# Performance work log

Measured on AMD Instinct MI355X. Metric: run time of the kernel, lower is better.

Reference implementation:

```python
import jax, jax.numpy as jnp
import numpy as np

B, C, L = 8, 256, 8192
G, K = 64, 7  # weight channels (groups) and kernel size


def setup_inputs() -> dict:
    key = jax.random.key(0)
    k1, k2 = jax.random.split(key)
    x = jax.random.normal(k1, (B, C, L), dtype=jnp.float32)
    w = jax.random.normal(k2, (B, G, K, L), dtype=jnp.float32)
    return {"x": x, "w": w}


def reference(x, w):
    # x: [B, C, L]; w: [B, G, K, L]
    Bsz, Cin, Len = x.shape
    Gw, Ks = w.shape[1], w.shape[2]
    pad = (Ks - 1) // 2
    x_pad = jnp.pad(x, ((0, 0), (0, 0), (pad, pad)))  # zero pad, 'same' output
    # x_unfold[b, c, k, l] = x_pad[b, c, l + k]  -> [B, C, K, L]
    x_unfold = jnp.stack([x_pad[:, :, k:k + Len] for k in range(Ks)], axis=2)
    # each input channel c uses weight channel c % G (spatially adaptive kernel)
    group_idx = jnp.arange(Cin) % Gw
    w_exp = w[:, group_idx]  # [B, C, K, L]
    return (x_unfold * w_exp).sum(axis=2)  # [B, C, L]
```

## Files before the change

### kernel.cpp

```cpp
#include <hip/hip_runtime.h>


constexpr int Bn   = 8;
constexpr int Cn   = 256;
constexpr int Ln   = 8192;
constexpr int Gn   = 64;
constexpr int Kn   = 7;
constexpr int CPG  = Cn / Gn;
constexpr int LPT  = 4;
constexpr int BLOCK = 256;
constexpr int TILE_L = BLOCK * LPT;
constexpr int NTILE  = Ln / TILE_L;

__global__ __launch_bounds__(BLOCK) void ska1d_kernel(
    const float* __restrict__ x,
    const float* __restrict__ w,
    float* __restrict__ out)
{
    const int bid   = blockIdx.x;
    const int ltile = bid % NTILE;
    const int g     = (bid / NTILE) % Gn;
    const int b     = bid / (NTILE * Gn);
    const int l0    = ltile * TILE_L + threadIdx.x * LPT;

    const float* wbase = w + ((size_t)(b * Gn + g) * Kn) * Ln + l0;
    float wf[Kn][4];
#pragma unroll
    for (int k = 0; k < Kn; ++k) {
        float4 wv = *reinterpret_cast<const float4*>(wbase + (size_t)k * Ln);
        wf[k][0] = wv.x; wf[k][1] = wv.y; wf[k][2] = wv.z; wf[k][3] = wv.w;
    }

#pragma unroll
    for (int j = 0; j < CPG; ++j) {
        const int c = g + j * Gn;
        const float* xrow = x + ((size_t)(b * Cn + c)) * Ln;

        float4 va = (l0 >= 4)
                  ? *reinterpret_cast<const float4*>(xrow + l0 - 4)
                  : make_float4(0.f, 0.f, 0.f, 0.f);
        float4 vb = *reinterpret_cast<const float4*>(xrow + l0);
        float4 vc = (l0 + 4 < Ln)
                  ? *reinterpret_cast<const float4*>(xrow + l0 + 4)
                  : make_float4(0.f, 0.f, 0.f, 0.f);

        float xs[12];
        xs[0] = va.x; xs[1] = va.y; xs[2]  = va.z; xs[3]  = va.w;
        xs[4] = vb.x; xs[5] = vb.y; xs[6]  = vb.z; xs[7]  = vb.w;
        xs[8] = vc.x; xs[9] = vc.y; xs[10] = vc.z; xs[11] = vc.w;

        float4 o;
        float* op = &o.x;
#pragma unroll
        for (int i = 0; i < 4; ++i) {
            float acc = 0.f;
#pragma unroll
            for (int k = 0; k < Kn; ++k)
                acc = fmaf(xs[1 + i + k], wf[k][i], acc);
            op[i] = acc;
        }
        *reinterpret_cast<float4*>(out + ((size_t)(b * Cn + c)) * Ln + l0) = o;
    }
}

extern "C" void kernel_launch(void* const* d_in, const int* in_sizes, int n_in,
                              void* d_out, int out_size, void* d_ws, size_t ws_size,
                              hipStream_t stream)
{
    const float* x = (const float*)d_in[0];
    const float* w = (const float*)d_in[1];
    float* out     = (float*)d_out;

    const int grid = Bn * Gn * NTILE;
    ska1d_kernel<<<grid, BLOCK, 0, stream>>>(x, w, out);
}
```

Baseline: 226.3 us.

## Stream tiles through triple-buffered LDS with async global_load_lds pipeline

Each block now owns one (batch, group) pair and loops over all length tiles. Weights and the four channels' inputs for upcoming tiles are prefetched straight into a three-deep LDS ring with global_load_lds, and vmcnt waits plus barriers overlap loads with compute. Only the tile edges are fetched with ordinary global loads. The grid shrinks to 512 blocks, and the large LDS footprint limits occupancy, so latency hiding depends on the hand-built pipeline rather than on many resident waves.

```diff
diff --git a/kernel.cpp b/kernel.cpp
--- a/kernel.cpp
+++ b/kernel.cpp
@@ -1,66 +1,140 @@
 #include <hip/hip_runtime.h>
 
 
-constexpr int Bn   = 8;
-constexpr int Cn   = 256;
-constexpr int Ln   = 8192;
-constexpr int Gn   = 64;
-constexpr int Kn   = 7;
-constexpr int CPG  = Cn / Gn;
-constexpr int LPT  = 4;
+constexpr int Bn = 8, Cn = 256, Ln = 8192, Gn = 64, Kn = 7;
 constexpr int BLOCK = 256;
-constexpr int TILE_L = BLOCK * LPT;
-constexpr int NTILE  = Ln / TILE_L;
+constexpr int TL    = 1024;
+constexpr int NT    = Ln / TL;
+constexpr int XOFF  = Kn * TL;
+constexpr int BUFF  = XOFF + 4 * TL;
+constexpr int NBUF  = 3;
+constexpr int UPW   = 11;
+
+__device__ __forceinline__ void stage1k(const float* gsrc, float* ldst, int lane) {
+    __builtin_amdgcn_global_load_lds(
+        (const __attribute__((address_space(1))) void*)(gsrc + lane * 4),
+        (__attribute__((address_space(3))) void*)ldst,
+        16, 0, 0);
+}
+
+__device__ __forceinline__ float4 ld4s(const float* p) {
+    return *reinterpret_cast<const float4*>(p);
+}
 
 __global__ __launch_bounds__(BLOCK) void ska1d_kernel(
     const float* __restrict__ x,
     const float* __restrict__ w,
     float* __restrict__ out)
 {
-    const int bid   = blockIdx.x;
-    const int ltile = bid % NTILE;
-    const int g     = (bid / NTILE) % Gn;
-    const int b     = bid / (NTILE * Gn);
-    const int l0    = ltile * TILE_L + threadIdx.x * LPT;
+    __shared__ float smem[NBUF * BUFF + 16];
 
-    const float* wbase = w + ((size_t)(b * Gn + g) * Kn) * Ln + l0;
-    float wf[Kn][4];
+    const int bid  = blockIdx.x;
+    const int g    = bid & (Gn - 1);
+    const int b    = bid >> 6;
+    const int tid  = (int)threadIdx.x;
+    const int wid  = tid >> 6;
+    const int lane = tid & 63;
+
+    const float* wg  = w + (size_t)(b * Gn + g) * Kn * Ln;
+    const float* xg0 = x + (size_t)(b * Cn + g) * Ln;
+    const float* xgw = xg0 + (size_t)wid * Gn * Ln;
+    float*       ogw = out + (size_t)(b * Cn + g) * Ln + (size_t)wid * Gn * Ln;
+
+    auto stage_tile = [&](int bufi, int t) {
+        const int T0 = t * TL;
+        float* buf = smem + bufi * BUFF;
 #pragma unroll
-    for (int k = 0; k < Kn; ++k) {
-        float4 wv = *reinterpret_cast<const float4*>(wbase + (size_t)k * Ln);
-        wf[k][0] = wv.x; wf[k][1] = wv.y; wf[k][2] = wv.z; wf[k][3] = wv.w;
+        for (int i = 0; i < UPW; ++i) {
+            const int u = wid * UPW + i;
+            const float* src;
+            int dst;
+            if (u < 28) {
+                const int k = u >> 2, q = u & 3;
+                src = wg + (size_t)k * Ln + T0 + q * 256;
+                dst = k * TL + q * 256;
+            } else {
+                const int v = u - 28;
+                const int j = v >> 2, q = v & 3;
+                src = xg0 + (size_t)j * Gn * Ln + T0 + q * 256;
+                dst = XOFF + j * TL + q * 256;
+            }
+            stage1k(src, buf + dst, lane);
+        }
+    };
+
+    auto edge_load = [&](int t, float4& eL, float4& eR) {
+        const int T0 = t * TL;
+        eL = make_float4(0.f, 0.f, 0.f, 0.f);
+        eR = eL;
+        if (lane == 0 && T0 > 0)
+            eL = *reinterpret_cast<const float4*>(xgw + T0 - 4);
+        if (lane == 63 && T0 + TL < Ln)
+            eR = *reinterpret_cast<const float4*>(xgw + T0 + TL);
+    };
+
+    auto compute_tile = [&](int bufi, int t, float4 eL, float4 eR) {
+        const int T0 = t * TL;
+        const float* wl = smem + bufi * BUFF;
+        const float* xl = wl + XOFF + wid * TL;
+#pragma unroll
+        for (int s = 0; s < 4; ++s) {
+            const int p = s * 256 + lane * 4;
+            float4 W0 = ld4s(wl + 0 * TL + p);
+            float4 W1 = ld4s(wl + 1 * TL + p);
+            float4 W2 = ld4s(wl + 2 * TL + p);
+            float4 W3 = ld4s(wl + 3 * TL + p);
+            float4 W4 = ld4s(wl + 4 * TL + p);
+            float4 W5 = ld4s(wl + 5 * TL + p);
+            float4 W6 = ld4s(wl + 6 * TL + p);
+            float4 va = (p >= 4)       ? ld4s(xl + p - 4) : eL;
+            float4 vb =                  ld4s(xl + p);
+            float4 vc = (p + 8 <= TL)  ? ld4s(xl + p + 4) : eR;
+
+            float xs[12];
+            xs[0] = va.x; xs[1] = va.y; xs[2]  = va.z; xs[3]  = va.w;
+            xs[4] = vb.x; xs[5] = vb.y; xs[6]  = vb.z; xs[7]  = vb.w;
+            xs[8] = vc.x; xs[9] = vc.y; xs[10] = vc.z; xs[11] = vc.w;
+
+            const float4 Wv[7] = {W0, W1, W2, W3, W4, W5, W6};
+            float4 o;
+            float* opx = &o.x;
+            const float* Wf = &Wv[0].x;
+#pragma unroll
+            for (int i = 0; i < 4; ++i) {
+                float acc = 0.f;
+#pragma unroll
+                for (int k = 0; k < Kn; ++k)
+                    acc = fmaf(xs[1 + i + k], Wf[k * 4 + i], acc);
+                opx[i] = acc;
+            }
+            *reinterpret_cast<float4*>(ogw + T0 + p) = o;
+        }
+    };
+
+    stage_tile(0, 0);
+    stage_tile(1, 1);
+    asm volatile("s_waitcnt vmcnt(11)" ::: "memory");
+    __builtin_amdgcn_sched_barrier(0);
+    __builtin_amdgcn_s_barrier();
+
+    float4 eL, eR;
+    for (int t = 0; t < NT - 2; ++t) {
+        edge_load(t, eL, eR);
+        __builtin_amdgcn_sched_barrier(0);
+        stage_tile((t + 2) % 3, t + 2);
+        __builtin_amdgcn_sched_barrier(0);
+        compute_tile(t % 3, t, eL, eR);
+        asm volatile("s_waitcnt vmcnt(11)" ::: "memory");
+        __builtin_amdgcn_sched_barrier(0);
+        __builtin_amdgcn_s_barrier();
     }
-
-#pragma unroll
-    for (int j = 0; j < CPG; ++j) {
-        const int c = g + j * Gn;
-        const float* xrow = x + ((size_t)(b * Cn + c)) * Ln;
-
-        float4 va = (l0 >= 4)
-                  ? *reinterpret_cast<const float4*>(xrow + l0 - 4)
-                  : make_float4(0.f, 0.f, 0.f, 0.f);
-        float4 vb = *reinterpret_cast<const float4*>(xrow + l0);
-        float4 vc = (l0 + 4 < Ln)
-                  ? *reinterpret_cast<const float4*>(xrow + l0 + 4)
-                  : make_float4(0.f, 0.f, 0.f, 0.f);
-
-        float xs[12];
-        xs[0] = va.x; xs[1] = va.y; xs[2]  = va.z; xs[3]  = va.w;
-        xs[4] = vb.x; xs[5] = vb.y; xs[6]  = vb.z; xs[7]  = vb.w;
-        xs[8] = vc.x; xs[9] = vc.y; xs[10] = vc.z; xs[11] = vc.w;
-
-        float4 o;
-        float* op = &o.x;
-#pragma unroll
-        for (int i = 0; i < 4; ++i) {
-            float acc = 0.f;
-#pragma unroll
-            for (int k = 0; k < Kn; ++k)
-                acc = fmaf(xs[1 + i + k], wf[k][i], acc);
-            op[i] = acc;
-        }
-        *reinterpret_cast<float4*>(out + ((size_t)(b * Cn + c)) * Ln + l0) = o;
-    }
+    edge_load(NT - 2, eL, eR);
+    compute_tile((NT - 2) % 3, NT - 2, eL, eR);
+    asm volatile("s_waitcnt vmcnt(0)" ::: "memory");
+    __builtin_amdgcn_sched_barrier(0);
+    __builtin_amdgcn_s_barrier();
+    edge_load(NT - 1, eL, eR);
+    compute_tile((NT - 1) % 3, NT - 1, eL, eR);
 }
 
 extern "C" void kernel_launch(void* const* d_in, const int* in_sizes, int n_in,
@@ -71,6 +145,6 @@
     const float* w = (const float*)d_in[1];
     float* out     = (float*)d_out;
 
-    const int grid = Bn * Gn * NTILE;
+    const int grid = Bn * Gn;
     ska1d_kernel<<<grid, BLOCK, 0, stream>>>(x, w, out);
 }
```

After: 235.3 us. +4.0%, slower.
